# Kernel tuning notes

Hardware: AMD Instinct MI355X
Metric: run time of the kernel (lower is better)

Reference implementation:

```python
import jax, jax.numpy as jnp
import numpy as np

B, T, D, H = 64, 196, 768, 3072
WBIT_MAX = 127.0          # int8 symmetric weight range
BIAS_MAX = 2.0 ** 31 - 1  # bias_bit = 32


def round_ste(v):
    # straight-through rounding (QAT semantics)
    return v + jax.lax.stop_gradient(jnp.round(v) - v)


def quant_linear(x, w, b, a_s, relu_clip):
    # symmetric per-tensor int8 weight quantization
    w_s = jnp.max(jnp.abs(w)) / WBIT_MAX
    w_int = jnp.clip(round_ste(w / w_s), -WBIT_MAX, WBIT_MAX)
    # bias quantized at the accumulator scale a_s * w_s (int32 range)
    b_int = jnp.clip(round_ste(b / (w_s * a_s)), -BIAS_MAX, BIAS_MAX)
    out = jnp.einsum('btd,hd->bth', x, w_int) + b_int  # integer-domain accumulation
    if relu_clip:
        out = jax.nn.relu(out)
    return out, w_s, a_s * w_s


def setup_inputs() -> dict:
    key = jax.random.key(0)
    ks = jax.random.split(key, 6)
    x = jnp.round(jax.random.normal(ks[0], (B, T, D), dtype=jnp.float32) * 20.0)  # int8-like activations
    w1 = jax.random.normal(ks[1], (H, D), dtype=jnp.float32) * 0.02
    b1 = jax.random.normal(ks[2], (H,), dtype=jnp.float32) * 0.02
    w2 = jax.random.normal(ks[3], (D, H), dtype=jnp.float32) * 0.02
    b2 = jax.random.normal(ks[4], (D,), dtype=jnp.float32) * 0.02
    a_s = jax.random.uniform(ks[5], (1,), dtype=jnp.float32, minval=0.01, maxval=0.05)
    return {"x": x, "w1": w1, "b1": b1, "w2": w2, "b2": b2, "a_s": a_s}


def reference(x, w1, b1, w2, b2, a_s):
    s = a_s[0]
    # fc1: quantized linear, no activation clip
    h, w_s1, s = quant_linear(x, w1, b1, s, relu_clip=False)
    # fc2: quantized linear with ReLU clip
    out, w_s2, s = quant_linear(h, w2, b2, s, relu_clip=True)
    return (out, s)
```

## Files before the change

### kernel.cpp

```cpp
#include <hip/hip_runtime.h>
#include <hip/hip_bf16.h>
#include <type_traits>

typedef __attribute__((ext_vector_type(4))) float f32x4;
typedef __attribute__((ext_vector_type(4))) int   i32x4;

static __device__ __forceinline__ void stage16(const void* g, void* l) {
  __builtin_amdgcn_global_load_lds((const __attribute__((address_space(1))) void*)g,
                                   (__attribute__((address_space(3))) void*)l,
                                   16, 0, 0);
}

__global__ void prep_kernel(const float4* __restrict__ x, uchar4* __restrict__ xq, int n4x,
                            const float4* __restrict__ w1, const float4* __restrict__ w2,
                            int n4w, unsigned* __restrict__ mx) {
  if (blockIdx.y == 0) {
    const int stride = gridDim.x * blockDim.x;
    for (int i = blockIdx.x * blockDim.x + threadIdx.x; i < n4x; i += stride) {
      float4 v = x[i];
      uchar4 o;
      o.x = (unsigned char)(char)fminf(fmaxf(v.x, -127.f), 127.f);
      o.y = (unsigned char)(char)fminf(fmaxf(v.y, -127.f), 127.f);
      o.z = (unsigned char)(char)fminf(fmaxf(v.z, -127.f), 127.f);
      o.w = (unsigned char)(char)fminf(fmaxf(v.w, -127.f), 127.f);
      xq[i] = o;
    }
  } else {
    if (blockIdx.x >= 96) return;
    __shared__ unsigned red[4];
    const float4* w = (blockIdx.y == 1) ? w1 : w2;
    unsigned m = 0;
    const int stride = 96 * 256;
    for (int i = blockIdx.x * blockDim.x + threadIdx.x; i < n4w; i += stride) {
      float4 v = w[i];
      unsigned a;
      a = __float_as_uint(fabsf(v.x)); m = m > a ? m : a;
      a = __float_as_uint(fabsf(v.y)); m = m > a ? m : a;
      a = __float_as_uint(fabsf(v.z)); m = m > a ? m : a;
      a = __float_as_uint(fabsf(v.w)); m = m > a ? m : a;
    }
#pragma unroll
    for (int off = 32; off > 0; off >>= 1) {
      unsigned t = (unsigned)__shfl_down((int)m, off, 64);
      m = m > t ? m : t;
    }
    if ((threadIdx.x & 63) == 0) red[threadIdx.x >> 6] = m;
    __syncthreads();
    if (threadIdx.x == 0) {
      unsigned t0 = red[0] > red[1] ? red[0] : red[1];
      unsigned t1 = red[2] > red[3] ? red[2] : red[3];
      atomicMax(mx + blockIdx.y - 1, t0 > t1 ? t0 : t1);
    }
  }
}

__global__ void quantwb_kernel(const float4* __restrict__ w1, const float4* __restrict__ w2,
                               uchar4* __restrict__ w1q, uchar4* __restrict__ w2q,
                               const float* __restrict__ b1, const float* __restrict__ b2,
                               float* __restrict__ b1i, float* __restrict__ b2i,
                               const unsigned* __restrict__ mx, const float* __restrict__ a_s,
                               float* __restrict__ s_out, int n4, int H, int D) {
  const float ws1 = __uint_as_float(mx[0]) / 127.0f;
  const float ws2 = __uint_as_float(mx[1]) / 127.0f;
  const int stride = gridDim.x * blockDim.x;
  if (blockIdx.y <= 1) {
    const float4* w = blockIdx.y ? w2 : w1;
    uchar4* wq = blockIdx.y ? w2q : w1q;
    const float ws = blockIdx.y ? ws2 : ws1;
    for (int i = blockIdx.x * blockDim.x + threadIdx.x; i < n4; i += stride) {
      float4 v = w[i];
      uchar4 o;
      o.x = (unsigned char)(char)fminf(fmaxf(rintf(v.x / ws), -127.f), 127.f);
      o.y = (unsigned char)(char)fminf(fmaxf(rintf(v.y / ws), -127.f), 127.f);
      o.z = (unsigned char)(char)fminf(fmaxf(rintf(v.z / ws), -127.f), 127.f);
      o.w = (unsigned char)(char)fminf(fmaxf(rintf(v.w / ws), -127.f), 127.f);
      wq[i] = o;
    }
  } else {
    if (blockIdx.x != 0) return;
    const float s0 = a_s[0];
    const float s1 = s0 * ws1;
    const float d1 = ws1 * s0;
    const float d2 = ws2 * s1;
    if (threadIdx.x == 0) s_out[0] = s1 * ws2;
    for (int i = threadIdx.x; i < H; i += blockDim.x) {
      float q = rintf(b1[i] / d1);
      b1i[i] = fminf(fmaxf(q, -2147483647.f), 2147483647.f);
    }
    for (int i = threadIdx.x; i < D; i += blockDim.x) {
      float q = rintf(b2[i] / d2);
      b2i[i] = fminf(fmaxf(q, -2147483647.f), 2147483647.f);
    }
  }
}


__global__ __launch_bounds__(256) void gemm_fc1(
    const char* __restrict__ A, const char* __restrict__ Bt,
    const float* __restrict__ b1f, unsigned char* __restrict__ hq,
    float* __restrict__ stab, int M, int N, int Kb)
{
  __shared__ char lds[2 * 32768 + 1024];
  const int tid = threadIdx.x;
  const int lane = tid & 63;
  const int wave = tid >> 6;
  const int wr = wave >> 1;
  const int wc = wave & 1;

  const int nbx = M / 128;
  const int nby = N / 128;
  const int bandSize = 16 * nby;
  const int b = blockIdx.x / bandSize;
  const int local = blockIdx.x - b * bandSize;
  const int r0 = b * 16;
  const int rn = min(16, nbx - r0);
  const int c = local / rn;
  const int r = r0 + (local - c * rn);
  const int row0 = r * 128;
  const int col0 = c * 128;

  const int srw = tid >> 3;
  const int chunk = (tid & 7) ^ (srw & 7);
  const char* Ag = A + (size_t)(row0 + srw) * Kb + chunk * 16;
  const char* Bg = Bt + (size_t)(col0 + srw) * Kb + chunk * 16;
  const int stA = wave * 1024;
  const int stB = 16384 + wave * 1024;

  auto stage = [&](int slot, int h) {
    const int hb = h << 7;
    char* da = lds + slot * 32768 + stA;
    char* db = lds + slot * 32768 + stB;
#pragma unroll
    for (int i = 0; i < 4; ++i)
      stage16(Ag + hb + (size_t)(i * 32) * Kb, da + i * 4096);
#pragma unroll
    for (int i = 0; i < 4; ++i)
      stage16(Bg + hb + (size_t)(i * 32) * Kb, db + i * 4096);
  };

  i32x4 acc[4][4];
#pragma unroll
  for (int i = 0; i < 4; ++i)
#pragma unroll
    for (int j = 0; j < 4; ++j) acc[i][j] = (i32x4)(0);

  const int nS = Kb >> 7;
  stage(0, 0);
  stage(1, 1);
  asm volatile("s_waitcnt vmcnt(8)" ::: "memory");
  __builtin_amdgcn_s_barrier();

  const int fr = lane & 15;
  const int fg = lane >> 4;
  const int xw = (fg ^ (fr & 7)) << 4;
  const int aoff = (wr * 64 + fr) * 128 + xw;
  const int boff = 16384 + (wc * 64 + fr) * 128 + xw;

  for (int t = 0; t < nS; ++t) {
    const int so = (t & 1) * 32768;
    i32x4 af[2][4], bf[2][4];
#pragma unroll
    for (int h = 0; h < 2; ++h) {
      const int hx = h << 6;
#pragma unroll
      for (int mi = 0; mi < 4; ++mi)
        af[h][mi] = *(const i32x4*)(lds + so + ((aoff ^ hx) + mi * 2048));
#pragma unroll
      for (int ni = 0; ni < 4; ++ni)
        bf[h][ni] = *(const i32x4*)(lds + so + ((boff ^ hx) + ni * 2048));
    }
    asm volatile("s_waitcnt lgkmcnt(0)" ::: "memory");
    __builtin_amdgcn_sched_barrier(0);
    __builtin_amdgcn_s_barrier();
    if (t + 2 < nS) stage(t & 1, t + 2);
    __builtin_amdgcn_s_setprio(1);
#pragma unroll
    for (int h = 0; h < 2; ++h)
#pragma unroll
      for (int mi = 0; mi < 4; ++mi)
#pragma unroll
        for (int ni = 0; ni < 4; ++ni)
          acc[mi][ni] = __builtin_amdgcn_mfma_i32_16x16x64_i8(
              af[h][mi], bf[h][ni], acc[mi][ni], 0, 0, 0);
    __builtin_amdgcn_s_setprio(0);
    if (t + 2 < nS) asm volatile("s_waitcnt vmcnt(8)" ::: "memory");
    else            asm volatile("s_waitcnt vmcnt(0)" ::: "memory");
    __builtin_amdgcn_s_barrier();
  }

  __syncthreads();
  unsigned char* ostage = (unsigned char*)lds;
  float* rowtab = (float*)(lds + 65536);
  const int orow_l = wr * 64 + fg * 4;
  const int ocol_l = wc * 64 + fr;
  float bv[4];
#pragma unroll
  for (int nf = 0; nf < 4; ++nf) bv[nf] = b1f[col0 + ocol_l + nf * 16];

#pragma unroll
  for (int mf = 0; mf < 4; ++mf) {
    float rmax[4] = {0.f, 0.f, 0.f, 0.f};
#pragma unroll
    for (int nf = 0; nf < 4; ++nf)
#pragma unroll
      for (int rg = 0; rg < 4; ++rg) {
        float v = (float)acc[mf][nf][rg] + bv[nf];
        rmax[rg] = fmaxf(rmax[rg], fabsf(v));
      }
#pragma unroll
    for (int rg = 0; rg < 4; ++rg) {
#pragma unroll
      for (int m = 1; m <= 8; m <<= 1)
        rmax[rg] = fmaxf(rmax[rg], __shfl_xor(rmax[rg], m, 64));
      if (fr == 0) rowtab[(orow_l + mf * 16 + rg) * 2 + wc] = rmax[rg];
    }
  }
  __syncthreads();
#pragma unroll
  for (int mf = 0; mf < 4; ++mf) {
#pragma unroll
    for (int rg = 0; rg < 4; ++rg) {
      const int lr = orow_l + mf * 16 + rg;
      float rm = fmaxf(rowtab[lr * 2], rowtab[lr * 2 + 1]);
      float inv = rm > 0.f ? 127.f / rm : 0.f;
      if (wc == 0 && fr == 0) stab[(size_t)(row0 + lr) * 24 + c] = rm * (1.f / 127.f);
#pragma unroll
      for (int nf = 0; nf < 4; ++nf) {
        float v = (float)acc[mf][nf][rg] + bv[nf];
        ostage[lr * 128 + ocol_l + nf * 16] = (unsigned char)(signed char)(int)rintf(v * inv);
      }
    }
  }
  __syncthreads();
#pragma unroll
  for (int v = 0; v < 4; ++v) {
    const int idx = tid + v * 256;
    const int lr = idx >> 3, cc = idx & 7;
    *(uint4*)(hq + (size_t)(row0 + lr) * N + col0 + cc * 16) =
        *(const uint4*)(ostage + lr * 128 + cc * 16);
  }
}

__global__ void requant_kernel(const uint4* __restrict__ hq, uint4* __restrict__ hq2,
                               const float* __restrict__ stab, float* __restrict__ srow,
                               int Mrows) {
  const int row = blockIdx.x * 4 + (threadIdx.x >> 6);
  if (row >= Mrows) return;
  const int lane = threadIdx.x & 63;
  const float* st = stab + (size_t)row * 24;
  float sr = 0.f;
#pragma unroll
  for (int i = 0; i < 24; ++i) sr = fmaxf(sr, st[i]);
  if (lane == 0) srow[row] = sr;
  const float rinv = sr > 0.f ? 1.f / sr : 0.f;
  const uint4* in = hq + (size_t)row * 192;
  uint4* outp = hq2 + (size_t)row * 192;
#pragma unroll
  for (int it = 0; it < 3; ++it) {
    const int j = lane + it * 64;
    const float ratio = st[j >> 3] * rinv;
    uint4 iv = in[j], ov;
    unsigned* ip = (unsigned*)&iv;
    unsigned* op = (unsigned*)&ov;
#pragma unroll
    for (int w = 0; w < 4; ++w) {
      unsigned rr = 0;
#pragma unroll
      for (int k = 0; k < 4; ++k) {
        int q = (int)(signed char)((ip[w] >> (k * 8)) & 0xFF);
        int nq = (int)rintf((float)q * ratio);
        rr |= ((unsigned)nq & 0xFF) << (k * 8);
      }
      op[w] = rr;
    }
    outp[j] = ov;
  }
}

__global__ __launch_bounds__(256) void gemm_fc2(
    const char* __restrict__ A, const char* __restrict__ Bt,
    const float* __restrict__ bias, const float* __restrict__ srow,
    float* __restrict__ Cout, int M, int N, int Kb)
{
  __shared__ char lds[2 * 32768];
  const int tid = threadIdx.x;
  const int lane = tid & 63;
  const int wave = tid >> 6;
  const int wr = wave >> 1;
  const int wc = wave & 1;

  const int nbx = M / 128;
  const int nby = N / 128;
  const int nwg = nbx * nby;
  const int q8 = nwg >> 3, r8 = nwg & 7;
  const int xcd = blockIdx.x & 7, bidx = blockIdx.x >> 3;
  const int wg = (xcd < r8 ? xcd * (q8 + 1) : r8 * (q8 + 1) + (xcd - r8) * q8) + bidx;
  const int r = wg / nby;
  const int c = wg % nby;
  const int row0 = r * 128;
  const int col0 = c * 128;

  const int srw = tid >> 3;
  const int chunk = (tid & 7) ^ (srw & 7);
  const char* Ag = A + (size_t)(row0 + srw) * Kb + chunk * 16;
  const char* Bg = Bt + (size_t)(col0 + srw) * Kb + chunk * 16;
  const int stA = wave * 1024;
  const int stB = 16384 + wave * 1024;

  auto stage = [&](int slot, int h) {
    const int hb = h << 7;
    char* da = lds + slot * 32768 + stA;
    char* db = lds + slot * 32768 + stB;
#pragma unroll
    for (int i = 0; i < 4; ++i)
      stage16(Ag + hb + (size_t)(i * 32) * Kb, da + i * 4096);
#pragma unroll
    for (int i = 0; i < 4; ++i)
      stage16(Bg + hb + (size_t)(i * 32) * Kb, db + i * 4096);
  };

  i32x4 acc[4][4];
#pragma unroll
  for (int i = 0; i < 4; ++i)
#pragma unroll
    for (int j = 0; j < 4; ++j) acc[i][j] = (i32x4)(0);

  const int nS = Kb >> 7;
  stage(0, 0);
  stage(1, 1);
  asm volatile("s_waitcnt vmcnt(8)" ::: "memory");
  __builtin_amdgcn_s_barrier();

  const int fr = lane & 15;
  const int fg = lane >> 4;
  const int xw = (fg ^ (fr & 7)) << 4;
  const int aoff = (wr * 64 + fr) * 128 + xw;
  const int boff = 16384 + (wc * 64 + fr) * 128 + xw;

  for (int t = 0; t < nS; ++t) {
    const int so = (t & 1) * 32768;
    i32x4 af[2][4], bf[2][4];
#pragma unroll
    for (int h = 0; h < 2; ++h) {
      const int hx = h << 6;
#pragma unroll
      for (int mi = 0; mi < 4; ++mi)
        af[h][mi] = *(const i32x4*)(lds + so + ((aoff ^ hx) + mi * 2048));
#pragma unroll
      for (int ni = 0; ni < 4; ++ni)
        bf[h][ni] = *(const i32x4*)(lds + so + ((boff ^ hx) + ni * 2048));
    }
    asm volatile("s_waitcnt lgkmcnt(0)" ::: "memory");
    __builtin_amdgcn_sched_barrier(0);
    __builtin_amdgcn_s_barrier();
    if (t + 2 < nS) stage(t & 1, t + 2);
    __builtin_amdgcn_s_setprio(1);
#pragma unroll
    for (int h = 0; h < 2; ++h)
#pragma unroll
      for (int mi = 0; mi < 4; ++mi)
#pragma unroll
        for (int ni = 0; ni < 4; ++ni)
          acc[mi][ni] = __builtin_amdgcn_mfma_i32_16x16x64_i8(
              af[h][mi], bf[h][ni], acc[mi][ni], 0, 0, 0);
    __builtin_amdgcn_s_setprio(0);
    if (t + 2 < nS) asm volatile("s_waitcnt vmcnt(8)" ::: "memory");
    else            asm volatile("s_waitcnt vmcnt(0)" ::: "memory");
    __builtin_amdgcn_s_barrier();
  }

  const int orow = row0 + wr * 64 + fg * 4;
  const int ocol = col0 + wc * 64 + fr;
#pragma unroll
  for (int mi = 0; mi < 4; ++mi) {
    float sr[4];
#pragma unroll
    for (int rg = 0; rg < 4; ++rg) sr[rg] = srow[orow + mi * 16 + rg];
#pragma unroll
    for (int ni = 0; ni < 4; ++ni) {
      const int col = ocol + ni * 16;
      const float bv = bias[col];
#pragma unroll
      for (int rg = 0; rg < 4; ++rg) {
        float v = sr[rg] * (float)acc[mi][ni][rg] + bv;
        Cout[(size_t)(orow + mi * 16 + rg) * N + col] = fmaxf(v, 0.f);
      }
    }
  }
}


extern "C" void kernel_launch(void* const* d_in, const int* in_sizes, int n_in,
                              void* d_out, int out_size, void* d_ws, size_t ws_size,
                              hipStream_t stream) {
  const float* x  = (const float*)d_in[0];
  const float* w1 = (const float*)d_in[1];
  const float* b1 = (const float*)d_in[2];
  const float* w2 = (const float*)d_in[3];
  const float* b2 = (const float*)d_in[4];
  const float* as = (const float*)d_in[5];

  const int Mrows = 64 * 196;
  const int D = 768, H = 3072;

  char* ws = (char*)d_ws;
  size_t off = 0;
  auto align256 = [](size_t v) { return (v + 255) & ~(size_t)255; };
  unsigned* mx = (unsigned*)(ws + off); off += 256;
  char* xq8    = (char*)(ws + off);     off += align256((size_t)Mrows * D);
  char* w1q8   = (char*)(ws + off);     off += align256((size_t)H * D);
  char* w2q8   = (char*)(ws + off);     off += align256((size_t)D * H);
  float* b1i = (float*)(ws + off); off += align256((size_t)H * 4);
  float* b2i = (float*)(ws + off); off += align256((size_t)D * 4);
  float* stab = (float*)(ws + off); off += align256((size_t)Mrows * 24 * 4);
  float* srow = (float*)(ws + off); off += align256((size_t)Mrows * 4);
  unsigned char* hq  = (unsigned char*)(ws + off); off += align256((size_t)Mrows * H);
  unsigned char* hq2 = (unsigned char*)(ws + off); off += align256((size_t)Mrows * H);
  if (off > ws_size) return;

  float* out = (float*)d_out;
  float* s_out = out + (out_size - 1);

  hipMemsetAsync(mx, 0, 8, stream);

  const int nw4 = H * D / 4;
  prep_kernel<<<dim3(1024, 3), dim3(256), 0, stream>>>(
      (const float4*)x, (uchar4*)xq8, Mrows * D / 4,
      (const float4*)w1, (const float4*)w2, nw4, mx);
  quantwb_kernel<<<dim3(1024, 3), dim3(256), 0, stream>>>(
      (const float4*)w1, (const float4*)w2, (uchar4*)w1q8, (uchar4*)w2q8,
      b1, b2, b1i, b2i, mx, as, s_out, nw4, H, D);

  gemm_fc1<<<dim3((Mrows / 128) * (H / 128)), dim3(256), 0, stream>>>(
      xq8, w1q8, b1i, hq, stab, Mrows, H, D);
  requant_kernel<<<dim3(Mrows / 4), dim3(256), 0, stream>>>(
      (const uint4*)hq, (uint4*)hq2, stab, srow, Mrows);
  gemm_fc2<<<dim3((Mrows / 128) * (D / 128)), dim3(256), 0, stream>>>(
      (const char*)hq2, w2q8, b2i, srow, out, Mrows, D, H);
}
```

Measured before the change: 148.9 us.

## Store fc1 output in permuted K layout and pre-permute w2 to match

The fc1 epilogue now packs each lane's four column fragments into one 32-bit word and writes it straight to global memory. This drops the LDS staging buffer and its extra barrier. The hidden activation's K dimension therefore lands in a permuted order within each 64-wide group, so the w2 quantization writes w2 with the same permutation and the fc2 dot products stay correct. It adds scattered 4-byte global stores in place of coalesced 16-byte rows, and w2 quantization now does strided scalar loads.

```diff
diff --git a/kernel.cpp b/kernel.cpp
--- a/kernel.cpp
+++ b/kernel.cpp
@@ -54,8 +54,8 @@
   }
 }
 
-__global__ void quantwb_kernel(const float4* __restrict__ w1, const float4* __restrict__ w2,
-                               uchar4* __restrict__ w1q, uchar4* __restrict__ w2q,
+__global__ void quantwb_kernel(const float* __restrict__ w1, const float* __restrict__ w2,
+                               unsigned char* __restrict__ w1q, unsigned* __restrict__ w2qw,
                                const float* __restrict__ b1, const float* __restrict__ b2,
                                float* __restrict__ b1i, float* __restrict__ b2i,
                                const unsigned* __restrict__ mx, const float* __restrict__ a_s,
@@ -63,18 +63,34 @@
   const float ws1 = __uint_as_float(mx[0]) / 127.0f;
   const float ws2 = __uint_as_float(mx[1]) / 127.0f;
   const int stride = gridDim.x * blockDim.x;
-  if (blockIdx.y <= 1) {
-    const float4* w = blockIdx.y ? w2 : w1;
-    uchar4* wq = blockIdx.y ? w2q : w1q;
-    const float ws = blockIdx.y ? ws2 : ws1;
+  if (blockIdx.y == 0) {
+    const float4* w = (const float4*)w1;
+    uchar4* wq = (uchar4*)w1q;
     for (int i = blockIdx.x * blockDim.x + threadIdx.x; i < n4; i += stride) {
       float4 v = w[i];
       uchar4 o;
-      o.x = (unsigned char)(char)fminf(fmaxf(rintf(v.x / ws), -127.f), 127.f);
-      o.y = (unsigned char)(char)fminf(fmaxf(rintf(v.y / ws), -127.f), 127.f);
-      o.z = (unsigned char)(char)fminf(fmaxf(rintf(v.z / ws), -127.f), 127.f);
-      o.w = (unsigned char)(char)fminf(fmaxf(rintf(v.w / ws), -127.f), 127.f);
+      o.x = (unsigned char)(char)fminf(fmaxf(rintf(v.x / ws1), -127.f), 127.f);
+      o.y = (unsigned char)(char)fminf(fmaxf(rintf(v.y / ws1), -127.f), 127.f);
+      o.z = (unsigned char)(char)fminf(fmaxf(rintf(v.z / ws1), -127.f), 127.f);
+      o.w = (unsigned char)(char)fminf(fmaxf(rintf(v.w / ws1), -127.f), 127.f);
       wq[i] = o;
+    }
+  } else if (blockIdx.y == 1) {
+    const int ndw = n4;
+    const int dpr = H >> 2;
+    for (int g = blockIdx.x * blockDim.x + threadIdx.x; g < ndw; g += stride) {
+      const int n = g / dpr;
+      const int d = g - n * dpr;
+      const int grp = d >> 4, dl = d & 15;
+      const float* src = w2 + (size_t)n * H + grp * 64 + dl;
+      unsigned r = 0;
+#pragma unroll
+      for (int i = 0; i < 4; ++i) {
+        float v = src[i * 16];
+        int q = (int)fminf(fmaxf(rintf(v / ws2), -127.f), 127.f);
+        r |= ((unsigned)q & 0xFFu) << (i * 8);
+      }
+      w2qw[g] = r;
     }
   } else {
     if (blockIdx.x != 0) return;
@@ -100,7 +116,7 @@
     const float* __restrict__ b1f, unsigned char* __restrict__ hq,
     float* __restrict__ stab, int M, int N, int Kb)
 {
-  __shared__ char lds[2 * 32768 + 1024];
+  __shared__ char lds[2 * 32768];
   const int tid = threadIdx.x;
   const int lane = tid & 63;
   const int wave = tid >> 6;
@@ -189,8 +205,7 @@
   }
 
   __syncthreads();
-  unsigned char* ostage = (unsigned char*)lds;
-  float* rowtab = (float*)(lds + 65536);
+  float* rowtab = (float*)lds;
   const int orow_l = wr * 64 + fg * 4;
   const int ocol_l = wc * 64 + fr;
   float bv[4];
@@ -224,20 +239,15 @@
       float rm = fmaxf(rowtab[lr * 2], rowtab[lr * 2 + 1]);
       float inv = rm > 0.f ? 127.f / rm : 0.f;
       if (wc == 0 && fr == 0) stab[(size_t)(row0 + lr) * 24 + c] = rm * (1.f / 127.f);
+      unsigned pk = 0;
 #pragma unroll
       for (int nf = 0; nf < 4; ++nf) {
         float v = (float)acc[mf][nf][rg] + bv[nf];
-        ostage[lr * 128 + ocol_l + nf * 16] = (unsigned char)(signed char)(int)rintf(v * inv);
+        int q = (int)rintf(v * inv);
+        pk |= ((unsigned)q & 0xFFu) << (nf * 8);
       }
-    }
-  }
-  __syncthreads();
-#pragma unroll
-  for (int v = 0; v < 4; ++v) {
-    const int idx = tid + v * 256;
-    const int lr = idx >> 3, cc = idx & 7;
-    *(uint4*)(hq + (size_t)(row0 + lr) * N + col0 + cc * 16) =
-        *(const uint4*)(ostage + lr * 128 + cc * 16);
+      *(unsigned*)(hq + (size_t)(row0 + lr) * N + col0 + wc * 64 + fr * 4) = pk;
+    }
   }
 }
 
@@ -428,7 +438,7 @@
       (const float4*)x, (uchar4*)xq8, Mrows * D / 4,
       (const float4*)w1, (const float4*)w2, nw4, mx);
   quantwb_kernel<<<dim3(1024, 3), dim3(256), 0, stream>>>(
-      (const float4*)w1, (const float4*)w2, (uchar4*)w1q8, (uchar4*)w2q8,
+      w1, w2, (unsigned char*)w1q8, (unsigned*)w2q8,
       b1, b2, b1i, b2i, mx, as, s_out, nw4, H, D);
 
   gemm_fc1<<<dim3((Mrows / 128) * (H / 128)), dim3(256), 0, stream>>>(
```

Measured after the change: 147.2 us. About the same (-1.2%).
